# Kernel tuning notes

Measured on AMD Instinct MI355X. Metric: run time of the kernel, lower is better.

The kernel has to match this reference:

```python
import jax, jax.numpy as jnp
import numpy as np

EPS = 1e-05


def setup_inputs() -> dict:
    key = jax.random.key(0)
    kx, kw, kb, kg, kp, kq = jax.random.split(key, 6)
    B, S, D = 32, 1024, 1024
    x = jax.random.normal(kx, (B, S, D), dtype=jnp.float32)
    # Linear(input_size, input_size) params
    W = jax.random.normal(kw, (D, D), dtype=jnp.float32) / np.sqrt(D)
    b = jax.random.normal(kb, (D,), dtype=jnp.float32) * 0.01
    gold_opinion = jax.random.uniform(kg, (B, S, 5), dtype=jnp.float32)
    predict_opinion = jax.random.uniform(kp, (B, S, 5), dtype=jnp.float32)
    gold_prob = jax.random.uniform(kq, (), dtype=jnp.float32)
    return {"x": x, "W": W, "b": b, "gold_opinion": gold_opinion,
            "predict_opinion": predict_opinion, "gold_prob": gold_prob}


def reference(x, W, b, gold_opinion, predict_opinion, gold_prob):
    # x: [B, S, D]
    S = x.shape[-2]
    x_tran = jnp.einsum('bsd,ed->bse', x, W) + b           # Linear: x @ W^T + b
    weights = jnp.einsum('bsd,btd->bst', x_tran, x)        # QK^T -> [B, S, S]

    idx = jnp.arange(S)
    location = jnp.abs(idx[None, :] - idx[:, None]).astype(x.dtype)  # [S, S]
    weights = weights * (1.0 / (location + EPS))           # distance decay

    # use_opinion = True branch
    gold_op = gold_opinion[:, :, 1] + gold_opinion[:, :, 2]          # [B, S]
    pred_op = predict_opinion[:, :, 3] + predict_opinion[:, :, 4]    # [B, S]
    opinion_weights = gold_prob * gold_op + (1.0 - gold_prob) * pred_op
    weights = weights * opinion_weights[:, :, None]

    weights = jnp.exp(jnp.tanh(weights))                   # pseudo-softmax numerator
    off_diag = (location != 0).astype(weights.dtype)       # eye(S) == 0 mask
    weights = weights * off_diag
    weights = weights / (jnp.sum(weights, axis=-1, keepdims=True) + EPS)
    return jnp.einsum('bst,btd->bsd', weights, x)
```

## Files before the change

kernel.cpp:

```cpp
#include <hip/hip_runtime.h>

#define EPSF 1e-5f

typedef _Float16 f16x8 __attribute__((ext_vector_type(8)));
typedef float f32x4 __attribute__((ext_vector_type(4)));

__device__ __forceinline__ void gload_lds16(const _Float16* g, _Float16* l) {
  __builtin_amdgcn_global_load_lds(
      (const __attribute__((address_space(1))) unsigned int*)g,
      (__attribute__((address_space(3))) unsigned int*)l, 16, 0, 0);
}

__device__ __forceinline__ f16x8 cvt8(float4 a, float4 b) {
  f16x8 h;
  h[0] = (_Float16)a.x; h[1] = (_Float16)a.y; h[2] = (_Float16)a.z; h[3] = (_Float16)a.w;
  h[4] = (_Float16)b.x; h[5] = (_Float16)b.y; h[6] = (_Float16)b.z; h[7] = (_Float16)b.w;
  return h;
}

template <int N>
__device__ __forceinline__ void wait_vm() {
  if constexpr (N == 8) asm volatile("s_waitcnt vmcnt(8) lgkmcnt(0)" ::: "memory");
  else if constexpr (N == 4) asm volatile("s_waitcnt vmcnt(4) lgkmcnt(0)" ::: "memory");
  else asm volatile("s_waitcnt vmcnt(0) lgkmcnt(0)" ::: "memory");
}

__device__ __forceinline__ void barrier_fence() {
  __builtin_amdgcn_s_barrier();
  asm volatile("" ::: "memory");
}

__device__ __forceinline__ void gemm256_run(const _Float16* __restrict__ Ag,
                                            const _Float16* __restrict__ Bg,
                                            _Float16* lds, f32x4 (&acc)[8][4]) {
  const int tid = threadIdx.x;
  const int wave = tid >> 6, lane = tid & 63;
  const int wm = wave >> 2, wn = wave & 3;
  const int quad = lane >> 4, nl = lane & 15;
  const int srow = tid >> 2;
  const long arow = (long)srow * 1024 + (((tid & 3) ^ (srow & 3)) * 8);
  const int pq = (quad ^ (nl & 3)) * 8;

#pragma unroll
  for (int i = 0; i < 8; ++i)
#pragma unroll
    for (int j = 0; j < 4; ++j) acc[i][j] = (f32x4){0.f, 0.f, 0.f, 0.f};

#define STAGE_A(t)                                                     \
  {                                                                    \
    _Float16* lA_ = lds + ((t) & 3) * 16384;                           \
    const _Float16* ga_ = Ag + arow + (t) * 32;                        \
    gload_lds16(ga_, lA_ + wave * 512);                                \
    gload_lds16(ga_ + 128 * 1024, lA_ + 4096 + wave * 512);            \
  }
#define STAGE_B(t)                                                     \
  {                                                                    \
    _Float16* lB_ = lds + ((t) & 3) * 16384 + 8192;                    \
    const _Float16* gb_ = Bg + arow + (t) * 32;                        \
    gload_lds16(gb_, lB_ + wave * 512);                                \
    gload_lds16(gb_ + 128 * 1024, lB_ + 4096 + wave * 512);            \
  }
#define LDA(t, mq, af)                                                 \
  {                                                                    \
    const _Float16* p_ =                                               \
        lds + ((t) & 3) * 16384 + (wm * 128 + (mq) * 64 + nl) * 32 + pq; \
    _Pragma("unroll") for (int i_ = 0; i_ < 4; ++i_)                   \
        af[i_] = *(const f16x8*)(p_ + i_ * 512);                       \
  }
#define LDB(t, bf)                                                     \
  {                                                                    \
    const _Float16* p_ =                                               \
        lds + ((t) & 3) * 16384 + 8192 + (wn * 64 + nl) * 32 + pq;     \
    _Pragma("unroll") for (int i_ = 0; i_ < 4; ++i_)                   \
        bf[i_] = *(const f16x8*)(p_ + i_ * 512);                       \
  }
#define MMA(mq, af, bf)                                                \
  {                                                                    \
    __builtin_amdgcn_s_setprio(1);                                     \
    _Pragma("unroll") for (int i_ = 0; i_ < 4; ++i_)                   \
        _Pragma("unroll") for (int j_ = 0; j_ < 4; ++j_)               \
            acc[(mq) * 4 + i_][j_] = __builtin_amdgcn_mfma_f32_16x16x32_f16( \
                af[i_], bf[j_], acc[(mq) * 4 + i_][j_], 0, 0, 0);      \
    __builtin_amdgcn_s_setprio(0);                                     \
  }
#define TILE(t, STG)                                                   \
  {                                                                    \
    f16x8 af_[4], bf_[4];                                              \
    LDA(t, 0, af_);                                                    \
    LDB(t, bf_);                                                       \
    if (STG) STAGE_A((t) + 3);                                         \
    MMA(0, af_, bf_);                                                  \
    f16x8 af2_[4];                                                     \
    LDA(t, 1, af2_);                                                   \
    if (STG) STAGE_B((t) + 3);                                         \
    MMA(1, af2_, bf_);                                                 \
  }

  STAGE_A(0); STAGE_B(0);
  STAGE_A(1); STAGE_B(1);
  STAGE_A(2); STAGE_B(2);
  wait_vm<8>();
  barrier_fence();

#pragma unroll 4
  for (int t = 0; t < 28; ++t) {
    TILE(t, true);
    wait_vm<8>();
    barrier_fence();
  }
  TILE(28, true);
  wait_vm<8>(); barrier_fence();
  TILE(29, false);
  wait_vm<4>(); barrier_fence();
  TILE(30, false);
  wait_vm<0>(); barrier_fence();
  TILE(31, false);

#undef TILE
#undef MMA
#undef LDB
#undef LDA
#undef STAGE_B
#undef STAGE_A
}

__global__ void prep_opin_k(const float* __restrict__ gold, const float* __restrict__ pred,
                            const float* __restrict__ gprob, float* __restrict__ opin, int n) {
  int i = blockIdx.x * 256 + threadIdx.x;
  if (i >= n) return;
  float gp = gprob[0];
  float go = gold[i * 5 + 1] + gold[i * 5 + 2];
  float po = pred[i * 5 + 3] + pred[i * 5 + 4];
  opin[i] = gp * go + (1.0f - gp) * po;
}

__global__ __launch_bounds__(256) void prep_h_k(const float* __restrict__ src,
                                                _Float16* __restrict__ dst) {
  long i = ((long)blockIdx.x * 256 + threadIdx.x) * 8;
  float4 a = *(const float4*)(src + i);
  float4 b = *(const float4*)(src + i + 4);
  *(f16x8*)(dst + i) = cvt8(a, b);
}

__global__ __launch_bounds__(256) void prep_xt_k(const float* __restrict__ x,
                                                 _Float16* __restrict__ XhT) {
  const int d = blockIdx.x * 256 + threadIdx.x;
  const int ts = blockIdx.y * 64;
  const long base = (long)blockIdx.z * 1024;
#pragma unroll
  for (int tg = 0; tg < 4; ++tg) {
    int t0 = ts + tg * 16;
    const float* src = x + (base + t0) * 1024 + d;
    float v[16];
#pragma unroll
    for (int j = 0; j < 16; ++j) v[j] = src[j * 1024];
    f16x8 h0, h1;
#pragma unroll
    for (int j = 0; j < 8; ++j) { h0[j] = (_Float16)v[j]; h1[j] = (_Float16)v[8 + j]; }
    _Float16* dst = XhT + (base + d) * 1024 + t0;
    *(f16x8*)dst = h0;
    *(f16x8*)(dst + 8) = h1;
  }
}

__global__ __launch_bounds__(512, 2) void gemm12_k(const _Float16* __restrict__ Xh,
                                                   const _Float16* __restrict__ Wh,
                                                   const float* __restrict__ bias,
                                                   _Float16* __restrict__ XT) {
  __shared__ _Float16 lds[4 * 16384];
  const int lin = blockIdx.x;
  const int ii = lin >> 3;
  const int mt = (lin & 7) * 16 + (ii >> 2);
  const int nt = ii & 3;
  const long m0 = (long)mt * 256;
  const int n0 = nt * 256;

  f32x4 acc[8][4];
  gemm256_run(Xh + m0 * 1024, Wh + (long)n0 * 1024, lds, acc);

  const int tid = threadIdx.x;
  const int wave = tid >> 6, lane = tid & 63;
  const int wm = wave >> 2, wn = wave & 3;
  const int quad = lane >> 4, nl = lane & 15;
#pragma unroll
  for (int mi = 0; mi < 8; ++mi) {
    long gm = m0 + wm * 128 + mi * 16 + quad * 4;
#pragma unroll
    for (int ni = 0; ni < 4; ++ni) {
      int gn = n0 + wn * 64 + ni * 16 + nl;
      float bv = bias[gn];
#pragma unroll
      for (int r = 0; r < 4; ++r)
        XT[(gm + r) * 1024 + gn] = (_Float16)(acc[mi][ni][r] + bv);
    }
  }
}

__global__ __launch_bounds__(512, 2) void scores2_k(const _Float16* __restrict__ XT,
                                                    const _Float16* __restrict__ Xh,
                                                    const float* __restrict__ opin,
                                                    _Float16* __restrict__ P,
                                                    float* __restrict__ denom) {
  __shared__ _Float16 lds[4 * 16384];
  const int lin = blockIdx.x;
  const int ii = lin >> 3;
  const int b = (lin & 7) + 8 * (ii >> 4);
  const int tile = ii & 15;
  const int s0 = (tile >> 2) * 256;
  const int t0 = (tile & 3) * 256;
  const long base = (long)b * 1024;

  f32x4 acc[8][4];
  gemm256_run(XT + (base + s0) * 1024, Xh + (base + t0) * 1024, lds, acc);

  const int tid = threadIdx.x;
  const int wave = tid >> 6, lane = tid & 63;
  const int wm = wave >> 2, wn = wave & 3;
  const int quad = lane >> 4, nl = lane & 15;
#pragma unroll
  for (int mi = 0; mi < 8; ++mi) {
#pragma unroll
    for (int r = 0; r < 4; ++r) {
      int s = s0 + wm * 128 + mi * 16 + quad * 4 + r;
      float opv = opin[b * 1024 + s];
      float rs = 0.f;
#pragma unroll
      for (int ni = 0; ni < 4; ++ni) {
        int tc = t0 + wn * 64 + ni * 16 + nl;
        float loc = fabsf((float)(s - tc));
        float arg = acc[mi][ni][r] * (1.0f / (loc + EPSF)) * opv;
        float th = 1.f - 2.f / (__expf(2.f * arg) + 1.f);
        float p = __expf(th);
        if (s == tc) p = 0.f;
        P[(base + s) * 1024 + tc] = (_Float16)p;
        rs += p;
      }
      rs += __shfl_xor(rs, 1);
      rs += __shfl_xor(rs, 2);
      rs += __shfl_xor(rs, 4);
      rs += __shfl_xor(rs, 8);
      if (nl == 0) atomicAdd(&denom[b * 1024 + s], rs);
    }
  }
}

__global__ __launch_bounds__(512, 2) void pv2_k(const _Float16* __restrict__ P,
                                                const _Float16* __restrict__ XhT,
                                                const float* __restrict__ denom,
                                                float* __restrict__ out) {
  __shared__ _Float16 lds[4 * 16384];
  const int lin = blockIdx.x;
  const int ii = lin >> 3;
  const int b = (lin & 7) + 8 * (ii >> 4);
  const int tile = ii & 15;
  const int s0 = (tile >> 2) * 256;
  const int d0 = (tile & 3) * 256;
  const long base = (long)b * 1024;

  f32x4 acc[8][4];
  gemm256_run(P + (base + s0) * 1024, XhT + (base + d0) * 1024, lds, acc);

  const int tid = threadIdx.x;
  const int wave = tid >> 6, lane = tid & 63;
  const int wm = wave >> 2, wn = wave & 3;
  const int quad = lane >> 4, nl = lane & 15;
#pragma unroll
  for (int mi = 0; mi < 8; ++mi) {
#pragma unroll
    for (int r = 0; r < 4; ++r) {
      int s = s0 + wm * 128 + mi * 16 + quad * 4 + r;
      float inv = 1.0f / (denom[b * 1024 + s] + EPSF);
#pragma unroll
      for (int ni = 0; ni < 4; ++ni) {
        int d = d0 + wn * 64 + ni * 16 + nl;
        out[(base + s) * 1024 + d] = acc[mi][ni][r] * inv;
      }
    }
  }
}

__global__ __launch_bounds__(256) void gemm1_k(const _Float16* __restrict__ Xh,
                                               const float* __restrict__ Wt,
                                               const float* __restrict__ bias,
                                               _Float16* __restrict__ XT) {
  __shared__ _Float16 As[128 * 32];
  __shared__ _Float16 Bs[128 * 32];
  const int tid = threadIdx.x;
  const int wave = tid >> 6, lane = tid & 63;
  const int wm = wave >> 1, wn = wave & 1;
  const int quad = lane >> 4, nl = lane & 15;
  const long m0 = (long)blockIdx.y * 128;
  const int n0 = blockIdx.x * 128;

  f32x4 acc[4][4];
  f32x4 zero = {0.f, 0.f, 0.f, 0.f};
#pragma unroll
  for (int i = 0; i < 4; ++i)
#pragma unroll
    for (int j = 0; j < 4; ++j) acc[i][j] = zero;

  const int crow = tid >> 2;
  const int ckc = (tid & 3) * 8;

  for (int k0 = 0; k0 < 1024; k0 += 32) {
#pragma unroll
    for (int it = 0; it < 2; ++it) {
      int c = it * 256 + tid;
      gload_lds16(Xh + (m0 + (c >> 2)) * 1024 + k0 + (c & 3) * 8,
                  &As[(it * 256 + wave * 64) * 8]);
      int row = it * 64 + crow;
      const float* sb = Wt + (long)(n0 + row) * 1024 + k0 + ckc;
      float4 b0 = *(const float4*)sb;
      float4 b1 = *(const float4*)(sb + 4);
      *(f16x8*)&Bs[row * 32 + ckc] = cvt8(b0, b1);
    }
    __syncthreads();
    f16x8 af[4], bf[4];
#pragma unroll
    for (int mi = 0; mi < 4; ++mi)
      af[mi] = *(const f16x8*)&As[(wm * 64 + mi * 16 + nl) * 32 + quad * 8];
#pragma unroll
    for (int ni = 0; ni < 4; ++ni)
      bf[ni] = *(const f16x8*)&Bs[(wn * 64 + ni * 16 + nl) * 32 + quad * 8];
#pragma unroll
    for (int mi = 0; mi < 4; ++mi)
#pragma unroll
      for (int ni = 0; ni < 4; ++ni)
        acc[mi][ni] = __builtin_amdgcn_mfma_f32_16x16x32_f16(af[mi], bf[ni], acc[mi][ni], 0, 0, 0);
    __syncthreads();
  }

#pragma unroll
  for (int mi = 0; mi < 4; ++mi) {
    long gm = m0 + wm * 64 + mi * 16 + quad * 4;
#pragma unroll
    for (int ni = 0; ni < 4; ++ni) {
      int gn = n0 + wn * 64 + ni * 16 + nl;
      float bv = bias[gn];
#pragma unroll
      for (int r = 0; r < 4; ++r)
        XT[(gm + r) * 1024 + gn] = (_Float16)(acc[mi][ni][r] + bv);
    }
  }
}

__global__ __launch_bounds__(256) void scores_f_k(const _Float16* __restrict__ XT,
                                                  const _Float16* __restrict__ Xh,
                                                  const float* __restrict__ opin,
                                                  _Float16* __restrict__ P,
                                                  float* __restrict__ denom) {
  __shared__ _Float16 As[128 * 32];
  __shared__ _Float16 Bs[128 * 32];
  const int tid = threadIdx.x;
  const int wave = tid >> 6, lane = tid & 63;
  const int wm = wave >> 1, wn = wave & 1;
  const int quad = lane >> 4, nl = lane & 15;
  const int b = blockIdx.z;
  const int s0 = blockIdx.y * 128;
  const int t0 = blockIdx.x * 128;
  const long base = (long)b * 1024;

  f32x4 acc[4][4];
  f32x4 zero = {0.f, 0.f, 0.f, 0.f};
#pragma unroll
  for (int i = 0; i < 4; ++i)
#pragma unroll
    for (int j = 0; j < 4; ++j) acc[i][j] = zero;

  for (int k0 = 0; k0 < 1024; k0 += 32) {
#pragma unroll
    for (int it = 0; it < 2; ++it) {
      int c = it * 256 + tid;
      gload_lds16(XT + (base + s0 + (c >> 2)) * 1024 + k0 + (c & 3) * 8,
                  &As[(it * 256 + wave * 64) * 8]);
      gload_lds16(Xh + (base + t0 + (c >> 2)) * 1024 + k0 + (c & 3) * 8,
                  &Bs[(it * 256 + wave * 64) * 8]);
    }
    __syncthreads();
    f16x8 af[4], bf[4];
#pragma unroll
    for (int mi = 0; mi < 4; ++mi)
      af[mi] = *(const f16x8*)&As[(wm * 64 + mi * 16 + nl) * 32 + quad * 8];
#pragma unroll
    for (int ni = 0; ni < 4; ++ni)
      bf[ni] = *(const f16x8*)&Bs[(wn * 64 + ni * 16 + nl) * 32 + quad * 8];
#pragma unroll
    for (int mi = 0; mi < 4; ++mi)
#pragma unroll
      for (int ni = 0; ni < 4; ++ni)
        acc[mi][ni] = __builtin_amdgcn_mfma_f32_16x16x32_f16(af[mi], bf[ni], acc[mi][ni], 0, 0, 0);
    __syncthreads();
  }

#pragma unroll
  for (int mi = 0; mi < 4; ++mi) {
#pragma unroll
    for (int r = 0; r < 4; ++r) {
      int s = s0 + wm * 64 + mi * 16 + quad * 4 + r;
      float opv = opin[b * 1024 + s];
      float rs = 0.f;
#pragma unroll
      for (int ni = 0; ni < 4; ++ni) {
        int t = t0 + wn * 64 + ni * 16 + nl;
        float loc = fabsf((float)(s - t));
        float arg = acc[mi][ni][r] * (1.0f / (loc + EPSF)) * opv;
        float th = 1.f - 2.f / (__expf(2.f * arg) + 1.f);
        float p = __expf(th);
        if (s == t) p = 0.f;
        P[(base + s) * 1024 + t] = (_Float16)p;
        rs += p;
      }
      rs += __shfl_xor(rs, 1);
      rs += __shfl_xor(rs, 2);
      rs += __shfl_xor(rs, 4);
      rs += __shfl_xor(rs, 8);
      if (nl == 0) atomicAdd(&denom[b * 1024 + s], rs);
    }
  }
}

__global__ __launch_bounds__(256) void pv_k(const _Float16* __restrict__ P,
                                            const float* __restrict__ X,
                                            const float* __restrict__ denom,
                                            float* __restrict__ out) {
  __shared__ _Float16 As[128 * 32];
  __shared__ _Float16 BsT[128 * 40];
  const int tid = threadIdx.x;
  const int wave = tid >> 6, lane = tid & 63;
  const int wm = wave >> 1, wn = wave & 1;
  const int quad = lane >> 4, nl = lane & 15;
  const int b = blockIdx.z;
  const int s0 = blockIdx.y * 128;
  const int d0 = blockIdx.x * 128;
  const long base = (long)b * 1024;

  const int dcol = tid & 127;
  const int tg = tid >> 7;

  f32x4 acc[4][4];
  f32x4 zero = {0.f, 0.f, 0.f, 0.f};
#pragma unroll
  for (int i = 0; i < 4; ++i)
#pragma unroll
    for (int j = 0; j < 4; ++j) acc[i][j] = zero;

  for (int k0 = 0; k0 < 1024; k0 += 32) {
#pragma unroll
    for (int it = 0; it < 2; ++it) {
      int c = it * 256 + tid;
      gload_lds16(P + (base + s0 + (c >> 2)) * 1024 + k0 + (c & 3) * 8,
                  &As[(it * 256 + wave * 64) * 8]);
    }
    {
      const float* xb = X + (base + k0 + tg * 16) * 1024 + d0 + dcol;
      float v[16];
#pragma unroll
      for (int j = 0; j < 16; ++j) v[j] = xb[j * 1024];
      f16x8 h0, h1;
#pragma unroll
      for (int j = 0; j < 8; ++j) { h0[j] = (_Float16)v[j]; h1[j] = (_Float16)v[8 + j]; }
      *(f16x8*)&BsT[dcol * 40 + tg * 16] = h0;
      *(f16x8*)&BsT[dcol * 40 + tg * 16 + 8] = h1;
    }
    __syncthreads();
    f16x8 af[4], bf[4];
#pragma unroll
    for (int mi = 0; mi < 4; ++mi)
      af[mi] = *(const f16x8*)&As[(wm * 64 + mi * 16 + nl) * 32 + quad * 8];
#pragma unroll
    for (int ni = 0; ni < 4; ++ni)
      bf[ni] = *(const f16x8*)&BsT[(wn * 64 + ni * 16 + nl) * 40 + quad * 8];
#pragma unroll
    for (int mi = 0; mi < 4; ++mi)
#pragma unroll
      for (int ni = 0; ni < 4; ++ni)
        acc[mi][ni] = __builtin_amdgcn_mfma_f32_16x16x32_f16(af[mi], bf[ni], acc[mi][ni], 0, 0, 0);
    __syncthreads();
  }

#pragma unroll
  for (int mi = 0; mi < 4; ++mi) {
#pragma unroll
    for (int r = 0; r < 4; ++r) {
      int s = s0 + wm * 64 + mi * 16 + quad * 4 + r;
      float inv = 1.0f / (denom[b * 1024 + s] + EPSF);
#pragma unroll
      for (int ni = 0; ni < 4; ++ni) {
        int d = d0 + wn * 64 + ni * 16 + nl;
        out[(base + s) * 1024 + d] = acc[mi][ni][r] * inv;
      }
    }
  }
}

extern "C" void kernel_launch(void* const* d_in, const int* in_sizes, int n_in,
                              void* d_out, int out_size, void* d_ws, size_t ws_size,
                              hipStream_t stream) {
  (void)in_sizes; (void)n_in; (void)out_size;
  const int B = 32, S = 1024;
  const int BS = B * S;

  const float* x     = (const float*)d_in[0];
  const float* W     = (const float*)d_in[1];
  const float* bias  = (const float*)d_in[2];
  const float* gold  = (const float*)d_in[3];
  const float* pred  = (const float*)d_in[4];
  const float* gprob = (const float*)d_in[5];

  const size_t P_BYTES  = (size_t)BS * 1024 * sizeof(_Float16);
  const size_t XT_BYTES = P_BYTES;
  const size_t OPIN_B   = (size_t)BS * sizeof(float);
  const size_t WH_B     = (size_t)1024 * 1024 * sizeof(_Float16);
  const size_t NEED_BIG = P_BYTES + XT_BYTES + 2 * OPIN_B + WH_B;

  char* ws = (char*)d_ws;
  _Float16* P = (_Float16*)ws;
  const bool big = ws_size >= NEED_BIG;

  _Float16* XT = (_Float16*)d_out;
  _Float16* Xh = XT + (size_t)BS * 1024;
  float* out   = (float*)d_out;

  if (big) {
    _Float16* XhT = (_Float16*)(ws + P_BYTES);
    float* opin   = (float*)(ws + P_BYTES + XT_BYTES);
    float* denom  = opin + BS;
    _Float16* Wh  = (_Float16*)(ws + P_BYTES + XT_BYTES + 2 * OPIN_B);

    hipMemsetAsync(denom, 0, OPIN_B, stream);
    prep_opin_k<<<BS / 256, 256, 0, stream>>>(gold, pred, gprob, opin, BS);
    prep_h_k<<<(BS * 1024 / 8) / 256, 256, 0, stream>>>(x, Xh);
    prep_h_k<<<(1024 * 1024 / 8) / 256, 256, 0, stream>>>(W, Wh);
    prep_xt_k<<<dim3(4, 16, 32), 256, 0, stream>>>(x, XhT);
    gemm12_k<<<512, 512, 0, stream>>>(Xh, Wh, bias, XT);
    scores2_k<<<512, 512, 0, stream>>>(XT, Xh, opin, P, denom);
    pv2_k<<<512, 512, 0, stream>>>(P, XhT, denom, out);
  } else {
    float* opin  = (float*)(ws + P_BYTES);
    float* denom = opin + BS;

    hipMemsetAsync(denom, 0, OPIN_B, stream);
    prep_opin_k<<<BS / 256, 256, 0, stream>>>(gold, pred, gprob, opin, BS);
    prep_h_k<<<(BS * 1024 / 8) / 256, 256, 0, stream>>>(x, Xh);
    gemm1_k<<<dim3(8, 256), 256, 0, stream>>>(Xh, W, bias, XT);
    scores_f_k<<<dim3(8, 8, 32), 256, 0, stream>>>(XT, Xh, opin, P, denom);
    pv_k<<<dim3(8, 8, 32), 256, 0, stream>>>(P, x, denom, out);
  }
}
```

Baseline: 539.7 us.

## Restructure GEMM mainloop to double-buffered BK=64 with finer barrier interleaving; LDS-transpose prep

The shared 256x256 GEMM core moves from a 4-deep ring of K=32 stages to two buffers of K=64 tiles with an XOR swizzle. Global-to-LDS loads for the next tile are split into quarter chunks interleaved with four MFMA phases, each guarded by barriers and lgkm/vm waits. The aim is better overlap of loads with MFMA and fewer loop iterations, at the cost of many more barriers per tile and less prefetch depth. The x transpose kernel is also rewritten to use an LDS tile, giving coalesced reads and writes instead of strided global loads.

```diff
diff --git a/kernel.cpp b/kernel.cpp
--- a/kernel.cpp
+++ b/kernel.cpp
@@ -18,18 +18,6 @@
   return h;
 }
 
-template <int N>
-__device__ __forceinline__ void wait_vm() {
-  if constexpr (N == 8) asm volatile("s_waitcnt vmcnt(8) lgkmcnt(0)" ::: "memory");
-  else if constexpr (N == 4) asm volatile("s_waitcnt vmcnt(4) lgkmcnt(0)" ::: "memory");
-  else asm volatile("s_waitcnt vmcnt(0) lgkmcnt(0)" ::: "memory");
-}
-
-__device__ __forceinline__ void barrier_fence() {
-  __builtin_amdgcn_s_barrier();
-  asm volatile("" ::: "memory");
-}
-
 __device__ __forceinline__ void gemm256_run(const _Float16* __restrict__ Ag,
                                             const _Float16* __restrict__ Bg,
                                             _Float16* lds, f32x4 (&acc)[8][4]) {
@@ -37,91 +25,90 @@
   const int wave = tid >> 6, lane = tid & 63;
   const int wm = wave >> 2, wn = wave & 3;
   const int quad = lane >> 4, nl = lane & 15;
-  const int srow = tid >> 2;
-  const long arow = (long)srow * 1024 + (((tid & 3) ^ (srow & 3)) * 8);
-  const int pq = (quad ^ (nl & 3)) * 8;
+  const int swz = nl & 7;
+  const long stg_off = (long)(wave * 8 + (lane >> 3)) * 1024 +
+                       (((lane & 7) ^ (lane >> 3)) * 8);
 
 #pragma unroll
   for (int i = 0; i < 8; ++i)
 #pragma unroll
     for (int j = 0; j < 4; ++j) acc[i][j] = (f32x4){0.f, 0.f, 0.f, 0.f};
 
-#define STAGE_A(t)                                                     \
-  {                                                                    \
-    _Float16* lA_ = lds + ((t) & 3) * 16384;                           \
-    const _Float16* ga_ = Ag + arow + (t) * 32;                        \
-    gload_lds16(ga_, lA_ + wave * 512);                                \
-    gload_lds16(ga_ + 128 * 1024, lA_ + 4096 + wave * 512);            \
-  }
-#define STAGE_B(t)                                                     \
-  {                                                                    \
-    _Float16* lB_ = lds + ((t) & 3) * 16384 + 8192;                    \
-    const _Float16* gb_ = Bg + arow + (t) * 32;                        \
-    gload_lds16(gb_, lB_ + wave * 512);                                \
-    gload_lds16(gb_ + 128 * 1024, lB_ + 4096 + wave * 512);            \
-  }
-#define LDA(t, mq, af)                                                 \
-  {                                                                    \
-    const _Float16* p_ =                                               \
-        lds + ((t) & 3) * 16384 + (wm * 128 + (mq) * 64 + nl) * 32 + pq; \
-    _Pragma("unroll") for (int i_ = 0; i_ < 4; ++i_)                   \
-        af[i_] = *(const f16x8*)(p_ + i_ * 512);                       \
-  }
-#define LDB(t, bf)                                                     \
-  {                                                                    \
-    const _Float16* p_ =                                               \
-        lds + ((t) & 3) * 16384 + 8192 + (wn * 64 + nl) * 32 + pq;     \
-    _Pragma("unroll") for (int i_ = 0; i_ < 4; ++i_)                   \
-        bf[i_] = *(const f16x8*)(p_ + i_ * 512);                       \
-  }
-#define MMA(mq, af, bf)                                                \
-  {                                                                    \
-    __builtin_amdgcn_s_setprio(1);                                     \
-    _Pragma("unroll") for (int i_ = 0; i_ < 4; ++i_)                   \
-        _Pragma("unroll") for (int j_ = 0; j_ < 4; ++j_)               \
+  f16x8 af[4], bf[4];
+
+#define STG(G, T1, q, isB)                                                   \
+  gload_lds16((G) + (long)(q) * 65536 + stg_off + (T1) * 64,                 \
+              lds + (((T1) & 1) * 32768 + (isB) * 16384 + (q) * 4096 + wave * 512))
+#define LDB4(bb, ksub)                                                       \
+  {                                                                          \
+    const _Float16* pB_ = lds + (bb) * 32768 + 16384 + (wn * 64 + nl) * 64 + \
+                          ((((ksub) * 4 + quad) ^ swz) * 8);                 \
+    _Pragma("unroll") for (int j_ = 0; j_ < 4; ++j_)                         \
+        bf[j_] = *(const f16x8*)(pB_ + j_ * 1024);                           \
+  }
+#define LDA4(bb, mq, ksub)                                                   \
+  {                                                                          \
+    const _Float16* pA_ = lds + (bb) * 32768 +                               \
+                          (wm * 128 + (mq) * 64 + nl) * 64 +                 \
+                          ((((ksub) * 4 + quad) ^ swz) * 8);                 \
+    _Pragma("unroll") for (int i_ = 0; i_ < 4; ++i_)                         \
+        af[i_] = *(const f16x8*)(pA_ + i_ * 1024);                           \
+  }
+#define MFMA16(mq)                                                           \
+  {                                                                          \
+    __builtin_amdgcn_s_setprio(1);                                           \
+    _Pragma("unroll") for (int i_ = 0; i_ < 4; ++i_)                         \
+        _Pragma("unroll") for (int j_ = 0; j_ < 4; ++j_)                     \
             acc[(mq) * 4 + i_][j_] = __builtin_amdgcn_mfma_f32_16x16x32_f16( \
-                af[i_], bf[j_], acc[(mq) * 4 + i_][j_], 0, 0, 0);      \
-    __builtin_amdgcn_s_setprio(0);                                     \
-  }
-#define TILE(t, STG)                                                   \
-  {                                                                    \
-    f16x8 af_[4], bf_[4];                                              \
-    LDA(t, 0, af_);                                                    \
-    LDB(t, bf_);                                                       \
-    if (STG) STAGE_A((t) + 3);                                         \
-    MMA(0, af_, bf_);                                                  \
-    f16x8 af2_[4];                                                     \
-    LDA(t, 1, af2_);                                                   \
-    if (STG) STAGE_B((t) + 3);                                         \
-    MMA(1, af2_, bf_);                                                 \
-  }
-
-  STAGE_A(0); STAGE_B(0);
-  STAGE_A(1); STAGE_B(1);
-  STAGE_A(2); STAGE_B(2);
-  wait_vm<8>();
-  barrier_fence();
-
-#pragma unroll 4
-  for (int t = 0; t < 28; ++t) {
-    TILE(t, true);
-    wait_vm<8>();
-    barrier_fence();
-  }
-  TILE(28, true);
-  wait_vm<8>(); barrier_fence();
-  TILE(29, false);
-  wait_vm<4>(); barrier_fence();
-  TILE(30, false);
-  wait_vm<0>(); barrier_fence();
-  TILE(31, false);
-
-#undef TILE
-#undef MMA
-#undef LDB
-#undef LDA
-#undef STAGE_B
-#undef STAGE_A
+                af[i_], bf[j_], acc[(mq) * 4 + i_][j_], 0, 0, 0);            \
+    __builtin_amdgcn_s_setprio(0);                                           \
+  }
+#define BAR __builtin_amdgcn_s_barrier()
+#define LGKM0 asm volatile("s_waitcnt lgkmcnt(0)" ::: "memory")
+#define VMW2 asm volatile("s_waitcnt vmcnt(2)" ::: "memory")
+#define VMW0 asm volatile("s_waitcnt vmcnt(0)" ::: "memory")
+
+  STG(Bg, 0, 0, 1); STG(Bg, 0, 1, 1);
+  STG(Ag, 0, 0, 0); STG(Ag, 0, 2, 0);
+  STG(Bg, 0, 2, 1); STG(Bg, 0, 3, 1);
+  STG(Ag, 0, 1, 0); STG(Ag, 0, 3, 0);
+  VMW2;
+  BAR;
+
+#pragma unroll 2
+  for (int T = 0; T < 15; ++T) {
+    const int bb = T & 1;
+    LDB4(bb, 0); LDA4(bb, 0, 0);
+    STG(Bg, T + 1, 0, 1); STG(Bg, T + 1, 1, 1);
+    BAR; LGKM0; MFMA16(0); VMW2; BAR;
+    LDA4(bb, 1, 0);
+    STG(Ag, T + 1, 0, 0); STG(Ag, T + 1, 2, 0);
+    BAR; LGKM0; MFMA16(1); BAR;
+    LDB4(bb, 1); LDA4(bb, 0, 1);
+    STG(Bg, T + 1, 2, 1); STG(Bg, T + 1, 3, 1);
+    BAR; LGKM0; MFMA16(0); BAR;
+    LDA4(bb, 1, 1);
+    STG(Ag, T + 1, 1, 0); STG(Ag, T + 1, 3, 0);
+    BAR; LGKM0; MFMA16(1); VMW2; BAR;
+  }
+  {
+    LDB4(1, 0); LDA4(1, 0, 0);
+    BAR; LGKM0; MFMA16(0); VMW0; BAR;
+    LDA4(1, 1, 0);
+    BAR; LGKM0; MFMA16(1); BAR;
+    LDB4(1, 1); LDA4(1, 0, 1);
+    BAR; LGKM0; MFMA16(0); BAR;
+    LDA4(1, 1, 1);
+    BAR; LGKM0; MFMA16(1); BAR;
+  }
+#undef VMW0
+#undef VMW2
+#undef LGKM0
+#undef BAR
+#undef MFMA16
+#undef LDA4
+#undef LDB4
+#undef STG
 }
 
 __global__ void prep_opin_k(const float* __restrict__ gold, const float* __restrict__ pred,
@@ -144,22 +131,20 @@
 
 __global__ __launch_bounds__(256) void prep_xt_k(const float* __restrict__ x,
                                                  _Float16* __restrict__ XhT) {
-  const int d = blockIdx.x * 256 + threadIdx.x;
-  const int ts = blockIdx.y * 64;
+  __shared__ _Float16 T[64][66];
+  const int d0 = blockIdx.x * 64, t0 = blockIdx.y * 64;
   const long base = (long)blockIdx.z * 1024;
-#pragma unroll
-  for (int tg = 0; tg < 4; ++tg) {
-    int t0 = ts + tg * 16;
-    const float* src = x + (base + t0) * 1024 + d;
-    float v[16];
-#pragma unroll
-    for (int j = 0; j < 16; ++j) v[j] = src[j * 1024];
-    f16x8 h0, h1;
-#pragma unroll
-    for (int j = 0; j < 8; ++j) { h0[j] = (_Float16)v[j]; h1[j] = (_Float16)v[8 + j]; }
-    _Float16* dst = XhT + (base + d) * 1024 + t0;
-    *(f16x8*)dst = h0;
-    *(f16x8*)(dst + 8) = h1;
+  const int c = threadIdx.x & 63, tr = threadIdx.x >> 6;
+#pragma unroll
+  for (int k = 0; k < 16; ++k) {
+    int t = k * 4 + tr;
+    T[t][c] = (_Float16)x[(base + t0 + t) * 1024 + d0 + c];
+  }
+  __syncthreads();
+#pragma unroll
+  for (int k = 0; k < 16; ++k) {
+    int d = k * 4 + tr;
+    XhT[(base + d0 + d) * 1024 + t0 + c] = T[c][d];
   }
 }
 
@@ -167,7 +152,7 @@
                                                    const _Float16* __restrict__ Wh,
                                                    const float* __restrict__ bias,
                                                    _Float16* __restrict__ XT) {
-  __shared__ _Float16 lds[4 * 16384];
+  __shared__ _Float16 lds[2 * 32768];
   const int lin = blockIdx.x;
   const int ii = lin >> 3;
   const int mt = (lin & 7) * 16 + (ii >> 2);
@@ -201,7 +186,7 @@
                                                     const float* __restrict__ opin,
                                                     _Float16* __restrict__ P,
                                                     float* __restrict__ denom) {
-  __shared__ _Float16 lds[4 * 16384];
+  __shared__ _Float16 lds[2 * 32768];
   const int lin = blockIdx.x;
   const int ii = lin >> 3;
   const int b = (lin & 7) + 8 * (ii >> 4);
@@ -248,7 +233,7 @@
                                                 const _Float16* __restrict__ XhT,
                                                 const float* __restrict__ denom,
                                                 float* __restrict__ out) {
-  __shared__ _Float16 lds[4 * 16384];
+  __shared__ _Float16 lds[2 * 32768];
   const int lin = blockIdx.x;
   const int ii = lin >> 3;
   const int b = (lin & 7) + 8 * (ii >> 4);
@@ -531,7 +516,7 @@
     prep_opin_k<<<BS / 256, 256, 0, stream>>>(gold, pred, gprob, opin, BS);
     prep_h_k<<<(BS * 1024 / 8) / 256, 256, 0, stream>>>(x, Xh);
     prep_h_k<<<(1024 * 1024 / 8) / 256, 256, 0, stream>>>(W, Wh);
-    prep_xt_k<<<dim3(4, 16, 32), 256, 0, stream>>>(x, XhT);
+    prep_xt_k<<<dim3(16, 16, 32), 256, 0, stream>>>(x, XhT);
     gemm12_k<<<512, 512, 0, stream>>>(Xh, Wh, bias, XT);
     scores2_k<<<512, 512, 0, stream>>>(XT, Xh, opin, P, denom);
     pv2_k<<<512, 512, 0, stream>>>(P, XhT, denom, out);
```

New measurement: 513.0 us. -4.9%, faster.
